# Kernel tuning notes

Hardware: AMD Instinct MI355X
Metric: run time of the kernel (lower is better)

The kernel has to match this reference:

```python
import jax, jax.numpy as jnp
import numpy as np

EPS = 1e-6

def _ln(x, w, b):
    m = x.mean(-1, keepdims=True)
    v = ((x - m) ** 2).mean(-1, keepdims=True)
    return (x - m) / jnp.sqrt(v + EPS) * w + b

def setup_inputs() -> dict:
    key = jax.random.key(0)
    ks = jax.random.split(key, 16)
    N, P, C, M = 8192, 64, 128, 4096
    MW = M * P  # 262144 gathered tokens
    A, BL = 131072, 65536
    x = jax.random.normal(ks[0], (N, P, C), dtype=jnp.float32)
    index_window = jax.random.permutation(ks[1], N)[:M]
    index_partition = jax.random.permutation(ks[2], MW)
    perm2 = jax.random.permutation(ks[3], MW)
    asy_index = perm2[:A]
    blocked_index = perm2[A:A + BL]
    p = lambda k, sh: 0.02 * jax.random.normal(k, sh, dtype=jnp.float32)
    return {
        "x": x,
        "index_window": index_window,
        "index_partition": index_partition,
        "asy_index": asy_index,
        "blocked_index": blocked_index,
        "M": M,
        "B": N,
        "ln1_w": jnp.ones((C,), jnp.float32), "ln1_b": jnp.zeros((C,), jnp.float32),
        "qkv_w": p(ks[4], (C, 3 * C)), "qkv_b": jnp.zeros((3 * C,), jnp.float32),
        "proj_w": p(ks[5], (C, C)), "proj_b": jnp.zeros((C,), jnp.float32),
        "gamma1": jnp.full((C,), 1e-1, jnp.float32),
        "ln2_w": jnp.ones((C,), jnp.float32), "ln2_b": jnp.zeros((C,), jnp.float32),
        "mlp_w1": p(ks[6], (C, 4 * C)), "mlp_b1": jnp.zeros((4 * C,), jnp.float32),
        "mlp_w2": p(ks[7], (4 * C, C)), "mlp_b2": jnp.zeros((C,), jnp.float32),
        "gamma2": jnp.full((C,), 1e-1, jnp.float32),
    }

def reference(x, index_window, index_partition, asy_index, blocked_index, M, B,
              ln1_w, ln1_b, qkv_w, qkv_b, proj_w, proj_b, gamma1,
              ln2_w, ln2_b, mlp_w1, mlp_b1, mlp_w2, mlp_b2, gamma2):
    N, P, C = x.shape
    H, dh = 4, 32
    scale = dh ** -0.5
    MW = index_partition.shape[0]
    x = _ln(x, ln1_w, ln1_b)                      # first_norm over whole input
    X = x                                          # (N, P, C)
    xw = x[index_window].reshape(-1, C)            # gather windows -> (MW, C)
    XX = xw
    xa = _ln(xw[asy_index], ln1_w, ln1_b)          # second norm on asy tokens
    xw = xw.at[asy_index].set(xa)
    shortcut = xa                                  # (A, C)
    xp = xw[index_partition].reshape(M, -1, C)     # (M, P, C) attention groups
    qkv = (xp @ qkv_w + qkv_b).reshape(M, P, H, 3 * dh).transpose(0, 2, 1, 3)
    q, k, v = jnp.split(qkv, 3, axis=3)            # each (M, H, P, dh)
    attn = jnp.einsum('mhqd,mhkd->mhqk', q, k) * scale
    # scatter scores keyed by key-token into flat map, mask blocked keys, gather back
    am = jnp.zeros((MW, P, H), attn.dtype)
    am = am.at[index_partition].set(jnp.transpose(attn, (0, 3, 2, 1)).reshape(MW, P, H))
    am = am.at[blocked_index].set(-10000.0)
    attn = jnp.transpose(am[index_partition].reshape(M, P, P, H), (0, 3, 2, 1))
    attn = jax.nn.softmax(attn, axis=-1)
    o = jnp.einsum('mhqk,mhkd->mhqd', attn, v).transpose(0, 2, 1, 3).reshape(M, P, C)
    o = o @ proj_w + proj_b
    XX = XX.at[index_partition].set(o.reshape(-1, C))
    y = XX[asy_index]
    # sub_layers: [ls1, droppath(id), ln2, mlp, ls2, droppath(id)]
    y = y * gamma1                                 # i=0
    y = shortcut + y                               # i=1 residual
    shortcut = y
    y2 = _ln(y, ln2_w, ln2_b)                      # i=2
    y2 = jax.nn.gelu(y2 @ mlp_w1 + mlp_b1, approximate=False) @ mlp_w2 + mlp_b2  # i=3
    y2 = y2 * gamma2                               # i=4
    y = shortcut + y2                              # i=5 residual
    XX = XX.at[asy_index].set(y)
    XX = XX.at[blocked_index].set(X[index_window].reshape(-1, C)[blocked_index])
    X = X.at[index_window].set(XX.reshape(M, -1, C))
    return X
```

## Files before the change

kernel.cpp:

```cpp
#include <hip/hip_runtime.h>
#include <hip/hip_bf16.h>
#include <math.h>

#define N_   8192
#define P_   64
#define C_   128
#define M_   4096
#define MW_  (M_ * P_)
#define A_   131072
#define BL_  65536
#define NROWS_ (N_ * P_)
#define LNBLK_   (NROWS_ / 8)
#define PREPBLK_ (196608 / 256)
#define SETBLK_  (MW_ / 256)

typedef __attribute__((ext_vector_type(8))) __bf16 bf16x8;
typedef __attribute__((ext_vector_type(4))) float f32x4;
typedef __attribute__((ext_vector_type(2))) __bf16 bf16x2;

__device__ __forceinline__ float wave_sum(float v) {
#pragma unroll
  for (int o = 32; o > 0; o >>= 1) v += __shfl_xor(v, o, 64);
  return v;
}

__global__ __launch_bounds__(256) void k_scatter2(unsigned char* p,
                                                  const int* __restrict__ ia,
                                                  const int* __restrict__ ib) {
  int i = blockIdx.x * 256 + threadIdx.x;
  if (i < A_) p[ia[i]] = 1;
  else {
    int j = i - A_;
    if (j < BL_) p[ib[j]] = 2;
  }
}

__global__ __launch_bounds__(256) void k_ln_prep_set(
    const float* __restrict__ x,
    const float* __restrict__ w, const float* __restrict__ b,
    const float* __restrict__ qkvw, const float* __restrict__ projw,
    const float* __restrict__ w1, const float* __restrict__ w2,
    __bf16* __restrict__ qkvt, __bf16* __restrict__ projt,
    __bf16* __restrict__ w1t, __bf16* __restrict__ w2t,
    unsigned char* __restrict__ flags,
    float* __restrict__ out) {
  if (blockIdx.x >= LNBLK_) {
    int bx = blockIdx.x - LNBLK_;
    if (bx >= PREPBLK_) {
      int i = (bx - PREPBLK_) * 256 + threadIdx.x;
      flags[i] = 0;
      return;
    }
    int i = bx * 256 + threadIdx.x;
    if (i < 384 * 128) {
      int col = i >> 7, row = i & 127;
      qkvt[i] = (__bf16)qkvw[row * 384 + col];
    } else if (i < 384 * 128 + 128 * 128) {
      int j = i - 384 * 128;
      int col = j >> 7, row = j & 127;
      projt[j] = (__bf16)projw[row * 128 + col];
    } else if (i < 384 * 128 + 128 * 128 + 512 * 128) {
      int j = i - 384 * 128 - 128 * 128;
      int col = j >> 7, row = j & 127;
      w1t[j] = (__bf16)w1[row * 512 + col];
    } else {
      int j = i - 384 * 128 - 128 * 128 - 512 * 128;
      int col = j >> 9, row = j & 511;
      w2t[j] = (__bf16)w2[row * 128 + col];
    }
    return;
  }
  int hw = threadIdx.x >> 5, l = threadIdx.x & 31;
  size_t row = (size_t)blockIdx.x * 8 + hw;
  float4 v = ((const float4*)(x + row * 128))[l];
  float s = (v.x + v.y) + (v.z + v.w);
#pragma unroll
  for (int o = 1; o < 32; o <<= 1) s += __shfl_xor(s, o, 64);
  float mean = s * (1.0f / 128.0f);
  float d0 = v.x - mean, d1 = v.y - mean, d2 = v.z - mean, d3 = v.w - mean;
  float q = (d0 * d0 + d1 * d1) + (d2 * d2 + d3 * d3);
#pragma unroll
  for (int o = 1; o < 32; o <<= 1) q += __shfl_xor(q, o, 64);
  float inv = rsqrtf(q * (1.0f / 128.0f) + 1e-6f);
  float4 wv = ((const float4*)w)[l];
  float4 bv = ((const float4*)b)[l];
  float4 o4;
  o4.x = d0 * inv * wv.x + bv.x;
  o4.y = d1 * inv * wv.y + bv.y;
  o4.z = d2 * inv * wv.z + bv.z;
  o4.w = d3 * inv * wv.w + bv.w;
  ((float4*)(out + row * 128))[l] = o4;
}

__global__ __launch_bounds__(256, 3) void k_attn(
    const int* __restrict__ iw,
    const int* __restrict__ ip, const unsigned char* __restrict__ flags,
    const float* __restrict__ ln1w, const float* __restrict__ ln1b,
    const __bf16* __restrict__ qkvt, const float* __restrict__ qkvb,
    const __bf16* __restrict__ projt, const float* __restrict__ projb,
    float* out) {
  __shared__ __align__(16) __bf16 XV[64 * 132];
  __shared__ __align__(16) __bf16 scratch[4 * 4352];
  __shared__ int srow[64];
  __shared__ unsigned char fl[64];

  const int tid = threadIdx.x;
  const int w = tid >> 6, lane = tid & 63;
  const int quad = lane >> 4, cl = lane & 15;
  const int m = blockIdx.x;

  if (tid < 64) {
    int s = ip[(m << 6) + tid];
    fl[tid] = flags[s];
    srow[tid] = iw[s >> 6] * 64 + (s & 63);
  }
  __syncthreads();

  __bf16* Xs = XV;
  const float lw0 = ln1w[2 * lane], lw1 = ln1w[2 * lane + 1];
  const float lb0 = ln1b[2 * lane], lb1 = ln1b[2 * lane + 1];

  {
    float2 xv[16];
#pragma unroll
    for (int ii = 0; ii < 16; ++ii) {
      int r = w + 4 * ii;
      xv[ii] = ((const float2*)(out + (size_t)srow[r] * 128))[lane];
    }
#pragma unroll
    for (int ii = 0; ii < 16; ++ii) {
      int r = w + 4 * ii;
      float y0 = xv[ii].x, y1 = xv[ii].y;
      if (fl[r] == 1) {
        float mean = wave_sum(y0 + y1) * (1.0f / 128.0f);
        float d0 = y0 - mean, d1 = y1 - mean;
        float inv = rsqrtf(wave_sum(d0 * d0 + d1 * d1) * (1.0f / 128.0f) + 1e-6f);
        y0 = d0 * inv * lw0 + lb0;
        y1 = d1 * inv * lw1 + lb1;
      }
      bf16x2 p2;
      p2[0] = (__bf16)y0; p2[1] = (__bf16)y1;
      *(bf16x2*)&Xs[r * 132 + 2 * lane] = p2;
    }
  }
  __syncthreads();

  __bf16* wsc = scratch + w * 4352;
  __bf16* Qs  = wsc;
  __bf16* Ks  = wsc + 2176;
  __bf16* Vts = XV + w * 2112;
  __bf16* Ps  = wsc;
  __bf16* Os  = wsc;
  const int h = w;

  bf16x8 af[4][4];
#pragma unroll
  for (int mt = 0; mt < 4; ++mt)
#pragma unroll
    for (int kt = 0; kt < 4; ++kt)
      af[mt][kt] = *(const bf16x8*)&Xs[(mt * 16 + cl) * 132 + kt * 32 + quad * 8];
  __syncthreads();

#pragma unroll
  for (int t = 0; t < 3; ++t) {
#pragma unroll
    for (int nt = 0; nt < 2; ++nt) {
      int col = h * 96 + t * 32 + nt * 16 + cl;
      bf16x8 bfr[4];
#pragma unroll
      for (int kt = 0; kt < 4; ++kt)
        bfr[kt] = *(const bf16x8*)&qkvt[(size_t)col * 128 + kt * 32 + quad * 8];
      float bias = qkvb[col];
      __builtin_amdgcn_s_setprio(1);
#pragma unroll
      for (int mt = 0; mt < 4; ++mt) {
        f32x4 acc = {bias, bias, bias, bias};
#pragma unroll
        for (int kt = 0; kt < 4; ++kt)
          acc = __builtin_amdgcn_mfma_f32_16x16x32_bf16(af[mt][kt], bfr[kt], acc, 0, 0, 0);
        if (t == 0) {
#pragma unroll
          for (int r = 0; r < 4; ++r)
            Qs[(mt * 16 + quad * 4 + r) * 34 + nt * 16 + cl] = (__bf16)acc[r];
        } else if (t == 1) {
#pragma unroll
          for (int r = 0; r < 4; ++r)
            Ks[(mt * 16 + quad * 4 + r) * 34 + nt * 16 + cl] = (__bf16)acc[r];
        } else {
#pragma unroll
          for (int r = 0; r < 4; ++r)
            Vts[(nt * 16 + cl) * 66 + mt * 16 + quad * 4 + r] = (__bf16)acc[r];
        }
      }
      __builtin_amdgcn_s_setprio(0);
    }
  }

  f32x4 sc4[4][4];
  {
    bf16x8 bk[4];
#pragma unroll
    for (int nt = 0; nt < 4; ++nt)
      bk[nt] = *(const bf16x8*)&Ks[(nt * 16 + cl) * 34 + quad * 8];
    __builtin_amdgcn_s_setprio(1);
#pragma unroll
    for (int mt = 0; mt < 4; ++mt) {
      bf16x8 aq = *(const bf16x8*)&Qs[(mt * 16 + cl) * 34 + quad * 8];
#pragma unroll
      for (int nt = 0; nt < 4; ++nt) {
        f32x4 z = {0.f, 0.f, 0.f, 0.f};
        sc4[mt][nt] = __builtin_amdgcn_mfma_f32_16x16x32_bf16(aq, bk[nt], z, 0, 0, 0);
      }
    }
    __builtin_amdgcn_s_setprio(0);
  }
  const float scale = 0.17677669529663687f;
  bool blk[4];
#pragma unroll
  for (int nt = 0; nt < 4; ++nt) blk[nt] = (fl[nt * 16 + cl] == 2);
#pragma unroll
  for (int mt = 0; mt < 4; ++mt)
#pragma unroll
    for (int nt = 0; nt < 4; ++nt)
#pragma unroll
      for (int r = 0; r < 4; ++r) {
        float v = sc4[mt][nt][r];
        sc4[mt][nt][r] = blk[nt] ? -10000.0f : v * scale;
      }
#pragma unroll
  for (int mt = 0; mt < 4; ++mt) {
#pragma unroll
    for (int r = 0; r < 4; ++r) {
      float mx = fmaxf(fmaxf(sc4[mt][0][r], sc4[mt][1][r]),
                       fmaxf(sc4[mt][2][r], sc4[mt][3][r]));
#pragma unroll
      for (int off = 1; off < 16; off <<= 1) mx = fmaxf(mx, __shfl_xor(mx, off, 64));
      float e0 = __expf(sc4[mt][0][r] - mx);
      float e1 = __expf(sc4[mt][1][r] - mx);
      float e2 = __expf(sc4[mt][2][r] - mx);
      float e3 = __expf(sc4[mt][3][r] - mx);
      float sm = (e0 + e1) + (e2 + e3);
#pragma unroll
      for (int off = 1; off < 16; off <<= 1) sm += __shfl_xor(sm, off, 64);
      float inv = 1.0f / sm;
      int row = mt * 16 + quad * 4 + r;
      Ps[row * 68 +  0 + cl] = (__bf16)(e0 * inv);
      Ps[row * 68 + 16 + cl] = (__bf16)(e1 * inv);
      Ps[row * 68 + 32 + cl] = (__bf16)(e2 * inv);
      Ps[row * 68 + 48 + cl] = (__bf16)(e3 * inv);
    }
  }

  f32x4 oacc[4][2];
  {
    bf16x8 bv[2][2];
#pragma unroll
    for (int nt = 0; nt < 2; ++nt)
#pragma unroll
      for (int kt = 0; kt < 2; ++kt)
        bv[nt][kt] = *(const bf16x8*)&Vts[(nt * 16 + cl) * 66 + kt * 32 + quad * 8];
    __builtin_amdgcn_s_setprio(1);
#pragma unroll
    for (int mt = 0; mt < 4; ++mt) {
      bf16x8 ap0 = *(const bf16x8*)&Ps[(mt * 16 + cl) * 68 + quad * 8];
      bf16x8 ap1 = *(const bf16x8*)&Ps[(mt * 16 + cl) * 68 + 32 + quad * 8];
#pragma unroll
      for (int nt = 0; nt < 2; ++nt) {
        f32x4 z = {0.f, 0.f, 0.f, 0.f};
        z = __builtin_amdgcn_mfma_f32_16x16x32_bf16(ap0, bv[nt][0], z, 0, 0, 0);
        z = __builtin_amdgcn_mfma_f32_16x16x32_bf16(ap1, bv[nt][1], z, 0, 0, 0);
        oacc[mt][nt] = z;
      }
    }
    __builtin_amdgcn_s_setprio(0);
  }
#pragma unroll
  for (int mt = 0; mt < 4; ++mt)
#pragma unroll
    for (int nt = 0; nt < 2; ++nt)
#pragma unroll
      for (int r = 0; r < 4; ++r)
        Os[(mt * 16 + quad * 4 + r) * 36 + nt * 16 + cl] = (__bf16)oacc[mt][nt][r];
  __syncthreads();

  const int jw = w * 32;
#pragma unroll
  for (int mt = 0; mt < 4; ++mt) {
#pragma unroll
    for (int nt = 0; nt < 2; ++nt) {
      int col = jw + nt * 16 + cl;
      float pb = projb[col];
      f32x4 acc = {pb, pb, pb, pb};
#pragma unroll
      for (int kt = 0; kt < 4; ++kt) {
        const __bf16* op = scratch + kt * 4352;
        bf16x8 a = *(const bf16x8*)&op[(mt * 16 + cl) * 36 + quad * 8];
        bf16x8 bb = *(const bf16x8*)&projt[(size_t)col * 128 + kt * 32 + quad * 8];
        acc = __builtin_amdgcn_mfma_f32_16x16x32_bf16(a, bb, acc, 0, 0, 0);
      }
#pragma unroll
      for (int r = 0; r < 4; ++r) {
        int row = mt * 16 + quad * 4 + r;
        if (fl[row] != 2)
          out[(size_t)srow[row] * 128 + col] = acc[r];
      }
    }
  }
}

__global__ __launch_bounds__(256, 3) void k_mlp(
    const float* __restrict__ x, const int* __restrict__ iw,
    const int* __restrict__ ia,
    const float* __restrict__ ln1w, const float* __restrict__ ln1b,
    const float* __restrict__ g1,
    const float* __restrict__ ln2w, const float* __restrict__ ln2b,
    const __bf16* __restrict__ w1t, const float* __restrict__ b1,
    const __bf16* __restrict__ w2t, const float* __restrict__ b2,
    const float* __restrict__ g2,
    float* out) {
  __shared__ __align__(16) __bf16 y2s[128 * 136];
  __shared__ __align__(16) __bf16 hb[128 * 68];
  __shared__ int wrs[128];

  const int tid = threadIdx.x;
  const int w = tid >> 6, lane = tid & 63;
  const int quad = lane >> 4, cl = lane & 15;

  if (tid < 128) {
    int s = ia[(blockIdx.x << 7) + tid];
    wrs[tid] = iw[s >> 6] * 64 + (s & 63);
  }
  __syncthreads();

  const float lw0 = ln1w[2 * lane], lw1 = ln1w[2 * lane + 1];
  const float lb0 = ln1b[2 * lane], lb1 = ln1b[2 * lane + 1];
  const float g1a = g1[2 * lane], g1b = g1[2 * lane + 1];
  const float l2w0 = ln2w[2 * lane], l2w1 = ln2w[2 * lane + 1];
  const float l2b0 = ln2b[2 * lane], l2b1 = ln2b[2 * lane + 1];

  for (int q = 0; q < 8; ++q) {
    float2 xv[4], ov[4];
#pragma unroll
    for (int ii = 0; ii < 4; ++ii) {
      int r = w + 4 * (q * 4 + ii);
      size_t wr = (size_t)wrs[r];
      xv[ii] = ((const float2*)(x + wr * 128))[lane];
      ov[ii] = ((const float2*)(out + wr * 128))[lane];
    }
#pragma unroll
    for (int ii = 0; ii < 4; ++ii) {
      int r = w + 4 * (q * 4 + ii);
      float mean = wave_sum(xv[ii].x + xv[ii].y) * (1.0f / 128.0f);
      float d0 = xv[ii].x - mean, d1 = xv[ii].y - mean;
      float inv = rsqrtf(wave_sum(d0 * d0 + d1 * d1) * (1.0f / 128.0f) + 1e-6f);
      float y0 = d0 * inv * lw0 + lb0, y1 = d1 * inv * lw1 + lb1;
      mean = wave_sum(y0 + y1) * (1.0f / 128.0f);
      d0 = y0 - mean; d1 = y1 - mean;
      inv = rsqrtf(wave_sum(d0 * d0 + d1 * d1) * (1.0f / 128.0f) + 1e-6f);
      float xa0 = d0 * inv * lw0 + lb0, xa1 = d1 * inv * lw1 + lb1;
      float yv0 = xa0 + g1a * ov[ii].x;
      float yv1 = xa1 + g1b * ov[ii].y;
      ((float2*)(out + (size_t)wrs[r] * 128))[lane] = make_float2(yv0, yv1);
      mean = wave_sum(yv0 + yv1) * (1.0f / 128.0f);
      d0 = yv0 - mean; d1 = yv1 - mean;
      inv = rsqrtf(wave_sum(d0 * d0 + d1 * d1) * (1.0f / 128.0f) + 1e-6f);
      bf16x2 p2;
      p2[0] = (__bf16)(d0 * inv * l2w0 + l2b0);
      p2[1] = (__bf16)(d1 * inv * l2w1 + l2b1);
      *(bf16x2*)&y2s[r * 136 + 2 * lane] = p2;
    }
  }
  __threadfence_block();
  __syncthreads();

  f32x4 zacc[8][2];
#pragma unroll
  for (int nt = 0; nt < 2; ++nt) {
    float bb = b2[w * 32 + nt * 16 + cl];
#pragma unroll
    for (int mt = 0; mt < 8; ++mt) zacc[mt][nt] = (f32x4){bb, bb, bb, bb};
  }

  for (int ch = 0; ch < 8; ++ch) {
    {
      int col = ch * 64 + w * 16 + cl;
      bf16x8 bfr[4];
#pragma unroll
      for (int kt = 0; kt < 4; ++kt)
        bfr[kt] = *(const bf16x8*)&w1t[(size_t)col * 128 + kt * 32 + quad * 8];
      float bias = b1[col];
      __builtin_amdgcn_s_setprio(1);
#pragma unroll
      for (int mt = 0; mt < 8; ++mt) {
        f32x4 acc = {bias, bias, bias, bias};
#pragma unroll
        for (int kt = 0; kt < 4; ++kt) {
          bf16x8 a = *(const bf16x8*)&y2s[(mt * 16 + cl) * 136 + kt * 32 + quad * 8];
          acc = __builtin_amdgcn_mfma_f32_16x16x32_bf16(a, bfr[kt], acc, 0, 0, 0);
        }
#pragma unroll
        for (int r = 0; r < 4; ++r) {
          float a = acc[r];
          float g = a * 0.5f * (1.0f + erff(a * 0.70710678118654752f));
          hb[(mt * 16 + quad * 4 + r) * 68 + w * 16 + cl] = (__bf16)g;
        }
      }
      __builtin_amdgcn_s_setprio(0);
    }
    __syncthreads();
#pragma unroll
    for (int nt = 0; nt < 2; ++nt) {
      int col = w * 32 + nt * 16 + cl;
      bf16x8 bfr[2];
#pragma unroll
      for (int kk = 0; kk < 2; ++kk)
        bfr[kk] = *(const bf16x8*)&w2t[(size_t)col * 512 + ch * 64 + kk * 32 + quad * 8];
      __builtin_amdgcn_s_setprio(1);
#pragma unroll
      for (int mt = 0; mt < 8; ++mt)
#pragma unroll
        for (int kk = 0; kk < 2; ++kk) {
          bf16x8 a = *(const bf16x8*)&hb[(mt * 16 + cl) * 68 + kk * 32 + quad * 8];
          zacc[mt][nt] = __builtin_amdgcn_mfma_f32_16x16x32_bf16(a, bfr[kk],
                                                                zacc[mt][nt], 0, 0, 0);
        }
      __builtin_amdgcn_s_setprio(0);
    }
    __syncthreads();
  }

#pragma unroll
  for (int mt = 0; mt < 8; ++mt)
#pragma unroll
    for (int nt = 0; nt < 2; ++nt) {
      int col = w * 32 + nt * 16 + cl;
      float gg = g2[col];
#pragma unroll
      for (int r = 0; r < 4; ++r) {
        int row = mt * 16 + quad * 4 + r;
        size_t a = (size_t)wrs[row] * 128 + col;
        out[a] = out[a] + gg * zacc[mt][nt][r];
      }
    }
}

extern "C" void kernel_launch(void* const* d_in, const int* in_sizes, int n_in,
                              void* d_out, int out_size, void* d_ws, size_t ws_size,
                              hipStream_t stream) {
  const float* x = (const float*)d_in[0];
  const int* iw = (const int*)d_in[1];
  const int* ip = (const int*)d_in[2];
  const int* ia = (const int*)d_in[3];
  const int* ib = (const int*)d_in[4];
  const float* ln1w = (const float*)d_in[7];
  const float* ln1b = (const float*)d_in[8];
  const float* qkvw = (const float*)d_in[9];
  const float* qkvb = (const float*)d_in[10];
  const float* projw = (const float*)d_in[11];
  const float* projb = (const float*)d_in[12];
  const float* g1 = (const float*)d_in[13];
  const float* ln2w = (const float*)d_in[14];
  const float* ln2b = (const float*)d_in[15];
  const float* w1 = (const float*)d_in[16];
  const float* b1 = (const float*)d_in[17];
  const float* w2 = (const float*)d_in[18];
  const float* b2 = (const float*)d_in[19];
  const float* g2 = (const float*)d_in[20];
  float* out = (float*)d_out;

  unsigned char* flags = (unsigned char*)d_ws;
  __bf16* qkvt = (__bf16*)((char*)d_ws + MW_);
  __bf16* projt = (__bf16*)((char*)d_ws + MW_ + 384 * 128 * 2);
  __bf16* w1t = (__bf16*)((char*)d_ws + MW_ + 384 * 128 * 2 + 128 * 128 * 2);
  __bf16* w2t = (__bf16*)((char*)d_ws + MW_ + 384 * 128 * 2 + 128 * 128 * 2 + 512 * 128 * 2);

  k_ln_prep_set<<<LNBLK_ + PREPBLK_ + SETBLK_, 256, 0, stream>>>(
      x, ln1w, ln1b, qkvw, projw, w1, w2, qkvt, projt, w1t, w2t, flags, out);
  k_scatter2<<<(A_ + BL_) / 256, 256, 0, stream>>>(flags, ia, ib);
  k_attn<<<M_, 256, 0, stream>>>(iw, ip, flags, ln1w, ln1b, qkvt, qkvb,
                                 projt, projb, out);
  k_mlp<<<A_ / 128, 256, 0, stream>>>(x, iw, ia, ln1w, ln1b, g1, ln2w, ln2b,
                                      w1t, b1, w2t, b2, g2, out);
}
```

Before: 836.2 us.

## Halve MLP row tile, raise occupancy, and vectorize LayerNorm loads to float4

The MLP kernel now handles 64 tokens per block instead of 128, with the grid doubled. This halves shared memory and accumulator registers so the launch bound can request 5 blocks per SM instead of 3. Both the attention-kernel and MLP-kernel LayerNorm stages now read rows as float4 with two rows per wave, reducing each row over 32 lanes with a half-wave shuffle sum. The costs are that each block reloads the MLP weights for half as many rows, and the tighter register budget may cause spills.

```diff
diff --git a/kernel.cpp b/kernel.cpp
--- a/kernel.cpp
+++ b/kernel.cpp
@@ -15,12 +15,18 @@
 #define SETBLK_  (MW_ / 256)
 
 typedef __attribute__((ext_vector_type(8))) __bf16 bf16x8;
+typedef __attribute__((ext_vector_type(4))) __bf16 bf16x4;
 typedef __attribute__((ext_vector_type(4))) float f32x4;
 typedef __attribute__((ext_vector_type(2))) __bf16 bf16x2;
 
 __device__ __forceinline__ float wave_sum(float v) {
 #pragma unroll
   for (int o = 32; o > 0; o >>= 1) v += __shfl_xor(v, o, 64);
+  return v;
+}
+__device__ __forceinline__ float half_sum(float v) {
+#pragma unroll
+  for (int o = 1; o < 32; o <<= 1) v += __shfl_xor(v, o, 64);
   return v;
 }
 
@@ -107,6 +113,7 @@
   const int tid = threadIdx.x;
   const int w = tid >> 6, lane = tid & 63;
   const int quad = lane >> 4, cl = lane & 15;
+  const int half = lane >> 5, l32 = lane & 31;
   const int m = blockIdx.x;
 
   if (tid < 64) {
@@ -117,30 +124,34 @@
   __syncthreads();
 
   __bf16* Xs = XV;
-  const float lw0 = ln1w[2 * lane], lw1 = ln1w[2 * lane + 1];
-  const float lb0 = ln1b[2 * lane], lb1 = ln1b[2 * lane + 1];
 
   {
-    float2 xv[16];
-#pragma unroll
-    for (int ii = 0; ii < 16; ++ii) {
-      int r = w + 4 * ii;
-      xv[ii] = ((const float2*)(out + (size_t)srow[r] * 128))[lane];
-    }
-#pragma unroll
-    for (int ii = 0; ii < 16; ++ii) {
-      int r = w + 4 * ii;
-      float y0 = xv[ii].x, y1 = xv[ii].y;
+    const float4 lw4 = ((const float4*)ln1w)[l32];
+    const float4 lb4 = ((const float4*)ln1b)[l32];
+    float4 xv[8];
+#pragma unroll
+    for (int ii = 0; ii < 8; ++ii) {
+      int r = w * 16 + ii * 2 + half;
+      xv[ii] = ((const float4*)(out + (size_t)srow[r] * 128))[l32];
+    }
+#pragma unroll
+    for (int ii = 0; ii < 8; ++ii) {
+      int r = w * 16 + ii * 2 + half;
+      float4 v = xv[ii];
       if (fl[r] == 1) {
-        float mean = wave_sum(y0 + y1) * (1.0f / 128.0f);
-        float d0 = y0 - mean, d1 = y1 - mean;
-        float inv = rsqrtf(wave_sum(d0 * d0 + d1 * d1) * (1.0f / 128.0f) + 1e-6f);
-        y0 = d0 * inv * lw0 + lb0;
-        y1 = d1 * inv * lw1 + lb1;
-      }
-      bf16x2 p2;
-      p2[0] = (__bf16)y0; p2[1] = (__bf16)y1;
-      *(bf16x2*)&Xs[r * 132 + 2 * lane] = p2;
+        float mean = half_sum((v.x + v.y) + (v.z + v.w)) * (1.0f / 128.0f);
+        float d0 = v.x - mean, d1 = v.y - mean, d2 = v.z - mean, d3 = v.w - mean;
+        float inv = rsqrtf(half_sum((d0 * d0 + d1 * d1) + (d2 * d2 + d3 * d3)) *
+                               (1.0f / 128.0f) + 1e-6f);
+        v.x = d0 * inv * lw4.x + lb4.x;
+        v.y = d1 * inv * lw4.y + lb4.y;
+        v.z = d2 * inv * lw4.z + lb4.z;
+        v.w = d3 * inv * lw4.w + lb4.w;
+      }
+      bf16x4 p4;
+      p4[0] = (__bf16)v.x; p4[1] = (__bf16)v.y;
+      p4[2] = (__bf16)v.z; p4[3] = (__bf16)v.w;
+      *(bf16x4*)&Xs[r * 132 + l32 * 4] = p4;
     }
   }
   __syncthreads();
@@ -308,7 +319,7 @@
   }
 }
 
-__global__ __launch_bounds__(256, 3) void k_mlp(
+__global__ __launch_bounds__(256, 5) void k_mlp(
     const float* __restrict__ x, const int* __restrict__ iw,
     const int* __restrict__ ia,
     const float* __restrict__ ln1w, const float* __restrict__ ln1b,
@@ -318,67 +329,79 @@
     const __bf16* __restrict__ w2t, const float* __restrict__ b2,
     const float* __restrict__ g2,
     float* out) {
-  __shared__ __align__(16) __bf16 y2s[128 * 136];
-  __shared__ __align__(16) __bf16 hb[128 * 68];
-  __shared__ int wrs[128];
+  __shared__ __align__(16) __bf16 y2s[64 * 136];
+  __shared__ __align__(16) __bf16 hb[64 * 68];
+  __shared__ int wrs[64];
 
   const int tid = threadIdx.x;
   const int w = tid >> 6, lane = tid & 63;
   const int quad = lane >> 4, cl = lane & 15;
-
-  if (tid < 128) {
-    int s = ia[(blockIdx.x << 7) + tid];
+  const int half = lane >> 5, l32 = lane & 31;
+
+  if (tid < 64) {
+    int s = ia[(blockIdx.x << 6) + tid];
     wrs[tid] = iw[s >> 6] * 64 + (s & 63);
   }
   __syncthreads();
 
-  const float lw0 = ln1w[2 * lane], lw1 = ln1w[2 * lane + 1];
-  const float lb0 = ln1b[2 * lane], lb1 = ln1b[2 * lane + 1];
-  const float g1a = g1[2 * lane], g1b = g1[2 * lane + 1];
-  const float l2w0 = ln2w[2 * lane], l2w1 = ln2w[2 * lane + 1];
-  const float l2b0 = ln2b[2 * lane], l2b1 = ln2b[2 * lane + 1];
-
-  for (int q = 0; q < 8; ++q) {
-    float2 xv[4], ov[4];
+  const float4 lw4 = ((const float4*)ln1w)[l32];
+  const float4 lb4 = ((const float4*)ln1b)[l32];
+  const float4 g14 = ((const float4*)g1)[l32];
+  const float4 l2w4 = ((const float4*)ln2w)[l32];
+  const float4 l2b4 = ((const float4*)ln2b)[l32];
+
+  for (int qb = 0; qb < 2; ++qb) {
+    float4 xv[4], ov[4];
 #pragma unroll
     for (int ii = 0; ii < 4; ++ii) {
-      int r = w + 4 * (q * 4 + ii);
+      int r = w * 16 + (qb * 4 + ii) * 2 + half;
       size_t wr = (size_t)wrs[r];
-      xv[ii] = ((const float2*)(x + wr * 128))[lane];
-      ov[ii] = ((const float2*)(out + wr * 128))[lane];
+      xv[ii] = ((const float4*)(x + wr * 128))[l32];
+      ov[ii] = ((const float4*)(out + wr * 128))[l32];
     }
 #pragma unroll
     for (int ii = 0; ii < 4; ++ii) {
-      int r = w + 4 * (q * 4 + ii);
-      float mean = wave_sum(xv[ii].x + xv[ii].y) * (1.0f / 128.0f);
-      float d0 = xv[ii].x - mean, d1 = xv[ii].y - mean;
-      float inv = rsqrtf(wave_sum(d0 * d0 + d1 * d1) * (1.0f / 128.0f) + 1e-6f);
-      float y0 = d0 * inv * lw0 + lb0, y1 = d1 * inv * lw1 + lb1;
-      mean = wave_sum(y0 + y1) * (1.0f / 128.0f);
-      d0 = y0 - mean; d1 = y1 - mean;
-      inv = rsqrtf(wave_sum(d0 * d0 + d1 * d1) * (1.0f / 128.0f) + 1e-6f);
-      float xa0 = d0 * inv * lw0 + lb0, xa1 = d1 * inv * lw1 + lb1;
-      float yv0 = xa0 + g1a * ov[ii].x;
-      float yv1 = xa1 + g1b * ov[ii].y;
-      ((float2*)(out + (size_t)wrs[r] * 128))[lane] = make_float2(yv0, yv1);
-      mean = wave_sum(yv0 + yv1) * (1.0f / 128.0f);
-      d0 = yv0 - mean; d1 = yv1 - mean;
-      inv = rsqrtf(wave_sum(d0 * d0 + d1 * d1) * (1.0f / 128.0f) + 1e-6f);
-      bf16x2 p2;
-      p2[0] = (__bf16)(d0 * inv * l2w0 + l2b0);
-      p2[1] = (__bf16)(d1 * inv * l2w1 + l2b1);
-      *(bf16x2*)&y2s[r * 136 + 2 * lane] = p2;
+      int r = w * 16 + (qb * 4 + ii) * 2 + half;
+      float4 v = xv[ii];
+      float mean = half_sum((v.x + v.y) + (v.z + v.w)) * (1.0f / 128.0f);
+      float d0 = v.x - mean, d1 = v.y - mean, d2 = v.z - mean, d3 = v.w - mean;
+      float inv = rsqrtf(half_sum((d0 * d0 + d1 * d1) + (d2 * d2 + d3 * d3)) *
+                             (1.0f / 128.0f) + 1e-6f);
+      float y0 = d0 * inv * lw4.x + lb4.x;
+      float y1 = d1 * inv * lw4.y + lb4.y;
+      float y2 = d2 * inv * lw4.z + lb4.z;
+      float y3 = d3 * inv * lw4.w + lb4.w;
+      mean = half_sum((y0 + y1) + (y2 + y3)) * (1.0f / 128.0f);
+      d0 = y0 - mean; d1 = y1 - mean; d2 = y2 - mean; d3 = y3 - mean;
+      inv = rsqrtf(half_sum((d0 * d0 + d1 * d1) + (d2 * d2 + d3 * d3)) *
+                       (1.0f / 128.0f) + 1e-6f);
+      float4 yv;
+      yv.x = (d0 * inv * lw4.x + lb4.x) + g14.x * ov[ii].x;
+      yv.y = (d1 * inv * lw4.y + lb4.y) + g14.y * ov[ii].y;
+      yv.z = (d2 * inv * lw4.z + lb4.z) + g14.z * ov[ii].z;
+      yv.w = (d3 * inv * lw4.w + lb4.w) + g14.w * ov[ii].w;
+      ((float4*)(out + (size_t)wrs[r] * 128))[l32] = yv;
+      mean = half_sum((yv.x + yv.y) + (yv.z + yv.w)) * (1.0f / 128.0f);
+      d0 = yv.x - mean; d1 = yv.y - mean; d2 = yv.z - mean; d3 = yv.w - mean;
+      inv = rsqrtf(half_sum((d0 * d0 + d1 * d1) + (d2 * d2 + d3 * d3)) *
+                       (1.0f / 128.0f) + 1e-6f);
+      bf16x4 p4;
+      p4[0] = (__bf16)(d0 * inv * l2w4.x + l2b4.x);
+      p4[1] = (__bf16)(d1 * inv * l2w4.y + l2b4.y);
+      p4[2] = (__bf16)(d2 * inv * l2w4.z + l2b4.z);
+      p4[3] = (__bf16)(d3 * inv * l2w4.w + l2b4.w);
+      *(bf16x4*)&y2s[r * 136 + l32 * 4] = p4;
     }
   }
   __threadfence_block();
   __syncthreads();
 
-  f32x4 zacc[8][2];
+  f32x4 zacc[4][2];
 #pragma unroll
   for (int nt = 0; nt < 2; ++nt) {
     float bb = b2[w * 32 + nt * 16 + cl];
 #pragma unroll
-    for (int mt = 0; mt < 8; ++mt) zacc[mt][nt] = (f32x4){bb, bb, bb, bb};
+    for (int mt = 0; mt < 4; ++mt) zacc[mt][nt] = (f32x4){bb, bb, bb, bb};
   }
 
   for (int ch = 0; ch < 8; ++ch) {
@@ -391,7 +414,7 @@
       float bias = b1[col];
       __builtin_amdgcn_s_setprio(1);
 #pragma unroll
-      for (int mt = 0; mt < 8; ++mt) {
+      for (int mt = 0; mt < 4; ++mt) {
         f32x4 acc = {bias, bias, bias, bias};
 #pragma unroll
         for (int kt = 0; kt < 4; ++kt) {
@@ -417,7 +440,7 @@
         bfr[kk] = *(const bf16x8*)&w2t[(size_t)col * 512 + ch * 64 + kk * 32 + quad * 8];
       __builtin_amdgcn_s_setprio(1);
 #pragma unroll
-      for (int mt = 0; mt < 8; ++mt)
+      for (int mt = 0; mt < 4; ++mt)
 #pragma unroll
         for (int kk = 0; kk < 2; ++kk) {
           bf16x8 a = *(const bf16x8*)&hb[(mt * 16 + cl) * 68 + kk * 32 + quad * 8];
@@ -430,7 +453,7 @@
   }
 
 #pragma unroll
-  for (int mt = 0; mt < 8; ++mt)
+  for (int mt = 0; mt < 4; ++mt)
 #pragma unroll
     for (int nt = 0; nt < 2; ++nt) {
       int col = w * 32 + nt * 16 + cl;
@@ -479,6 +502,6 @@
   k_scatter2<<<(A_ + BL_) / 256, 256, 0, stream>>>(flags, ia, ib);
   k_attn<<<M_, 256, 0, stream>>>(iw, ip, flags, ln1w, ln1b, qkvt, qkvb,
                                  projt, projb, out);
-  k_mlp<<<A_ / 128, 256, 0, stream>>>(x, iw, ia, ln1w, ln1b, g1, ln2w, ln2b,
-                                      w1t, b1, w2t, b2, g2, out);
-}
+  k_mlp<<<A_ / 64, 256, 0, stream>>>(x, iw, ia, ln1w, ln1b, g1, ln2w, ln2b,
+                                     w1t, b1, w2t, b2, g2, out);
+}
```

Result: faster. 770.6 us (median of 2 runs) (-7.8%).
